# Optimization experiments

Measured on AMD Instinct MI355X. Metric: run time of the kernel, lower is better.

Reference implementation:

```python
import jax, jax.numpy as jnp
import numpy as np

LN_EPS = 1e-12
BIG = 1e30
BAND = 15  # end index may be at most 15 tokens after start


def output_layer(x, w1, b1, g, b, w2, b2):
    # Linear -> ReLU -> LayerNorm -> Linear (dropout is identity at eval)
    h = jax.nn.relu(x @ w1 + b1)
    mu = jnp.mean(h, axis=-1, keepdims=True)
    var = jnp.mean(jnp.square(h - mu), axis=-1, keepdims=True)
    h = (h - mu) * jax.lax.rsqrt(var + LN_EPS) * g + b
    return h @ w2 + b2


def setup_inputs() -> dict:
    key = jax.random.key(0)
    ks = jax.random.split(key, 8)
    B, S, D = 8, 4096, 1024
    H2 = 2 * D
    inp = {
        "context_input": jax.random.normal(ks[0], (B, S, D), jnp.float32),
        "context_mask": jnp.ones((B, S), jnp.float32),
    }
    def head(k1, k2, n_ans):
        return (
            0.02 * jax.random.normal(k1, (D, H2), jnp.float32),
            jnp.zeros((H2,), jnp.float32),
            jnp.ones((H2,), jnp.float32),
            jnp.zeros((H2,), jnp.float32),
            0.02 * jax.random.normal(k2, (H2, n_ans), jnp.float32),
            jnp.zeros((n_ans,), jnp.float32),
        )
    for name, k1, k2, n_ans in [("start", ks[1], ks[2], 1), ("end", ks[3], ks[4], 1), ("type", ks[5], ks[6], 4)]:
        w1, b1, g, b, w2, b2 = head(k1, k2, n_ans)
        inp[f"{name}_w1"] = w1; inp[f"{name}_b1"] = b1
        inp[f"{name}_g"] = g; inp[f"{name}_b"] = b
        inp[f"{name}_w2"] = w2; inp[f"{name}_b2"] = b2
    return inp


def reference(context_input, context_mask,
              start_w1, start_b1, start_g, start_b, start_w2, start_b2,
              end_w1, end_b1, end_g, end_b, end_w2, end_b2,
              type_w1, type_b1, type_g, type_b, type_w2, type_b2):
    S = context_input.shape[1]
    start_pred = output_layer(context_input, start_w1, start_b1, start_g, start_b, start_w2, start_b2)[..., 0] \
        - BIG * (1.0 - context_mask)  # [B,S]
    end_pred = output_layer(context_input, end_w1, end_b1, end_g, end_b, end_w2, end_b2)[..., 0] \
        - BIG * (1.0 - context_mask)  # [B,S]
    type_pred = output_layer(context_input[:, 0, :], type_w1, type_b1, type_g, type_b, type_w2, type_b2)  # [B,4]

    # outer[b,i,j] = start[b,i] + end[b,j], masked to band 0 <= j-i <= 15
    outer = start_pred[:, :, None] + end_pred[:, None, :]  # [B,S,S]
    i = jnp.arange(S)[:, None]
    j = jnp.arange(S)[None, :]
    band = ((j >= i) & (j <= i + BAND)).astype(outer.dtype)  # [S,S]
    outer = outer - BIG * (1.0 - band)[None]

    yp1 = jnp.argmax(jnp.max(outer, axis=2), axis=1)  # best start index [B]
    yp2 = jnp.argmax(jnp.max(outer, axis=1), axis=1)  # best end index [B]
    return start_pred, end_pred, type_pred, yp1, yp2
```

## Files before the change

kernel.cpp:

```cpp
#include <hip/hip_runtime.h>

typedef _Float16 f16x8 __attribute__((ext_vector_type(8)));
typedef float f32x4 __attribute__((ext_vector_type(4)));

#define BIGF 1e30f
#define M_TOT 32768
#define H2 2048

#define WS_XH 0u
#define WS_WT 67108864u
#define WS_BVEC 75497472u
#define WS_GW2 75513856u
#define WS_CONSTS 75530240u
#define WS_PART 75530496u
#define WS_TPART 100696320u

__global__ void k_convert_x(const float* __restrict__ x, _Float16* __restrict__ xh) {
  size_t i = ((size_t)blockIdx.x * 256 + threadIdx.x) * 8;
  float4 v0 = *(const float4*)(x + i);
  float4 v1 = *(const float4*)(x + i + 4);
  f16x8 h;
  h[0] = (_Float16)v0.x; h[1] = (_Float16)v0.y; h[2] = (_Float16)v0.z; h[3] = (_Float16)v0.w;
  h[4] = (_Float16)v1.x; h[5] = (_Float16)v1.y; h[6] = (_Float16)v1.z; h[7] = (_Float16)v1.w;
  *(f16x8*)(xh + i) = h;
}

__global__ void k_convert_w(const float* __restrict__ w_s, const float* __restrict__ w_e,
                            _Float16* __restrict__ wt) {
  __shared__ float tile[64][65];
  const float* w = blockIdx.z ? w_e : w_s;
  int n0 = blockIdx.x * 64, k0 = blockIdx.y * 64;
  int tx = threadIdx.x & 63, ty = threadIdx.x >> 6;
#pragma unroll
  for (int i = ty; i < 64; i += 4) tile[i][tx] = w[(size_t)(k0 + i) * H2 + n0 + tx];
  __syncthreads();
#pragma unroll
  for (int i = ty; i < 64; i += 4) {
    wt[((size_t)(blockIdx.z * H2 + n0 + i)) * 1024 + k0 + tx] = (_Float16)tile[tx][i];
  }
}

__global__ void k_pack(const float* __restrict__ s_b1, const float* __restrict__ s_g,
                       const float* __restrict__ s_w2, const float* __restrict__ e_b1,
                       const float* __restrict__ e_g, const float* __restrict__ e_w2,
                       float* __restrict__ bvec, float* __restrict__ gw2) {
  int i = blockIdx.x * 256 + threadIdx.x;
  int head = i >> 11, j = i & (H2 - 1);
  bvec[i] = head ? e_b1[j] : s_b1[j];
  gw2[i] = head ? e_g[j] * e_w2[j] : s_g[j] * s_w2[j];
}

__global__ void k_consts(const float* __restrict__ s_g, const float* __restrict__ s_b,
                         const float* __restrict__ s_w2, const float* __restrict__ s_b2,
                         const float* __restrict__ e_g, const float* __restrict__ e_b,
                         const float* __restrict__ e_w2, const float* __restrict__ e_b2,
                         float* __restrict__ consts) {
  int h = blockIdx.x;
  const float* g = h ? e_g : s_g;
  const float* b = h ? e_b : s_b;
  const float* w2 = h ? e_w2 : s_w2;
  const float* b2 = h ? e_b2 : s_b2;
  float c1 = 0.f, c2 = 0.f;
  for (int j = threadIdx.x; j < H2; j += 256) {
    float w = w2[j];
    c1 += g[j] * w;
    c2 += b[j] * w;
  }
  for (int m = 1; m < 64; m <<= 1) { c1 += __shfl_xor(c1, m); c2 += __shfl_xor(c2, m); }
  __shared__ float r1[4], r2[4];
  int wid = threadIdx.x >> 6;
  if ((threadIdx.x & 63) == 0) { r1[wid] = c1; r2[wid] = c2; }
  __syncthreads();
  if (threadIdx.x == 0) {
    consts[h * 2 + 0] = r1[0] + r1[1] + r1[2] + r1[3];
    consts[h * 2 + 1] = r2[0] + r2[1] + r2[2] + r2[3] + b2[0];
  }
}

#define BUF 65536
#define STA(q, tile, bufo)                                                              \
  __builtin_amdgcn_global_load_lds(                                                     \
      (const __attribute__((address_space(1))) unsigned int*)(srcA + (size_t)(q) * 131072 + (size_t)(tile) * 128), \
      (__attribute__((address_space(3))) unsigned int*)(lds + (bufo) + (q) * 8192 + t * 16), 16, 0, 0)
#define STB(q, tile, bufo)                                                              \
  __builtin_amdgcn_global_load_lds(                                                     \
      (const __attribute__((address_space(1))) unsigned int*)(srcB + (size_t)(q) * 131072 + (size_t)(tile) * 128), \
      (__attribute__((address_space(3))) unsigned int*)(lds + (bufo) + 32768 + (q) * 8192 + t * 16), 16, 0, 0)

#define READA(AF, mi0, BUFO)                                                            \
  AF[0][0] = *(const f16x8*)(lds + (BUFO) + arow + (mi0) * 2048 + low0);                \
  AF[0][1] = *(const f16x8*)(lds + (BUFO) + arow + (mi0) * 2048 + low1);                \
  AF[1][0] = *(const f16x8*)(lds + (BUFO) + arow + ((mi0) + 1) * 2048 + low0);          \
  AF[1][1] = *(const f16x8*)(lds + (BUFO) + arow + ((mi0) + 1) * 2048 + low1);

#define READB(BF, BUFO)                                                                 \
  _Pragma("unroll")                                                                     \
  for (int nj = 0; nj < 4; ++nj) {                                                      \
    BF[nj][0] = *(const f16x8*)(lds + (BUFO) + brow + nj * 2048 + low0);                \
    BF[nj][1] = *(const f16x8*)(lds + (BUFO) + brow + nj * 2048 + low1);                \
  }

#define MFMA2(m0, m1, AF, BF)                                                           \
  __builtin_amdgcn_s_setprio(1);                                                        \
  _Pragma("unroll")                                                                     \
  for (int nj = 0; nj < 4; ++nj) {                                                      \
    acc[m0][nj] = __builtin_amdgcn_mfma_f32_16x16x32_f16(AF[0][0], BF[nj][0], acc[m0][nj], 0, 0, 0); \
    acc[m1][nj] = __builtin_amdgcn_mfma_f32_16x16x32_f16(AF[1][0], BF[nj][0], acc[m1][nj], 0, 0, 0); \
  }                                                                                     \
  _Pragma("unroll")                                                                     \
  for (int nj = 0; nj < 4; ++nj) {                                                      \
    acc[m0][nj] = __builtin_amdgcn_mfma_f32_16x16x32_f16(AF[0][1], BF[nj][1], acc[m0][nj], 0, 0, 0); \
    acc[m1][nj] = __builtin_amdgcn_mfma_f32_16x16x32_f16(AF[1][1], BF[nj][1], acc[m1][nj], 0, 0, 0); \
  }                                                                                     \
  __builtin_amdgcn_s_setprio(0);

#define K_ITER(g, OB, OBN, BFC, BFN)                                                    \
  {                                                                                     \
                           \
    READA(afB, 2, OB);                                                                  \
    if ((g) < 15) { STA(1, (g) + 1, OBN); STA(3, (g) + 1, OBN); }                       \
    asm volatile("s_waitcnt lgkmcnt(4)" ::: "memory");                                  \
    __builtin_amdgcn_s_barrier();                                                       \
    __builtin_amdgcn_sched_barrier(0);                                                  \
    MFMA2(0, 1, afA, BFC);                                                              \
                           \
    READA(afA, 4, OB);                                                                  \
    if ((g) < 14) { STB(0, (g) + 2, OB); STB(1, (g) + 2, OB); }                         \
    asm volatile("s_waitcnt lgkmcnt(4)" ::: "memory");                                  \
    __builtin_amdgcn_s_barrier();                                                       \
    __builtin_amdgcn_sched_barrier(0);                                                  \
    MFMA2(2, 3, afB, BFC);                                                              \
           \
    READA(afB, 6, OB);                                                                  \
    if ((g) < 14) { STB(2, (g) + 2, OB); STB(3, (g) + 2, OB); }                         \
    if ((g) < 14)       asm volatile("s_waitcnt vmcnt(4)" ::: "memory");                \
    else if ((g) == 14) asm volatile("s_waitcnt vmcnt(0)" ::: "memory");                \
    asm volatile("s_waitcnt lgkmcnt(4)" ::: "memory");                                  \
    __builtin_amdgcn_s_barrier();                                                       \
    __builtin_amdgcn_sched_barrier(0);                                                  \
    MFMA2(4, 5, afA, BFC);                                                              \
       \
    if ((g) < 15) {                                                                     \
      READB(BFN, OBN);                                                                  \
      READA(afA, 0, OBN);                                                               \
      if ((g) < 14) { STA(0, (g) + 2, OB); STA(2, (g) + 2, OB); }                       \
      asm volatile("s_waitcnt lgkmcnt(12)" ::: "memory");                               \
    } else {                                                                            \
      asm volatile("s_waitcnt lgkmcnt(0)" ::: "memory");                                \
    }                                                                                   \
    __builtin_amdgcn_s_barrier();                                                       \
    __builtin_amdgcn_sched_barrier(0);                                                  \
    MFMA2(6, 7, afB, BFC);                                                              \
  }

__global__ __launch_bounds__(512, 2) void k_gemm(const _Float16* __restrict__ Xh,
                                                 const _Float16* __restrict__ Wt,
                                                 const float* __restrict__ bvec,
                                                 const float* __restrict__ gw2,
                                                 float* __restrict__ partials) {
  __shared__ char lds[2 * BUF];
  const int nb = blockIdx.x;
  const int mb = blockIdx.y;
  const int t = threadIdx.x;
  const int lane = t & 63, wid = t >> 6;
  const int c15 = lane & 15, g4 = lane >> 4;
  const int wmg = wid >> 2;
  const int wn = (wid & 3) * 64;

  f32x4 acc[8][4];
#pragma unroll
  for (int i = 0; i < 8; ++i)
#pragma unroll
    for (int j = 0; j < 4; ++j) acc[i][j] = (f32x4){0.f, 0.f, 0.f, 0.f};

  const char* Abase = (const char*)(Xh + (size_t)mb * 256 * 1024);
  const char* Bbase = (const char*)(Wt + (size_t)nb * 256 * 1024);
  const int rowl = t >> 3;
  const int swz = ((t & 7) * 16) ^ ((rowl & 7) << 4);
  const char* srcA = Abase + (size_t)rowl * 2048 + swz;
  const char* srcB = Bbase + (size_t)rowl * 2048 + swz;

  const int xorv = (c15 & 7) << 4;
  const int low0 = (g4 * 16) ^ xorv;
  const int low1 = (64 + g4 * 16) ^ xorv;
  const int arow = (wmg * 128 + c15) * 128;
  const int brow = 32768 + (wn + c15) * 128;

  STA(0, 0, 0); STA(1, 0, 0); STA(2, 0, 0); STA(3, 0, 0);
  STB(0, 0, 0); STB(1, 0, 0); STB(2, 0, 0); STB(3, 0, 0);
  STB(0, 1, BUF); STB(1, 1, BUF); STB(2, 1, BUF); STB(3, 1, BUF);
  STA(0, 1, BUF); STA(2, 1, BUF);
  asm volatile("s_waitcnt vmcnt(6)" ::: "memory");
  __builtin_amdgcn_s_barrier();
  __builtin_amdgcn_sched_barrier(0);

  f16x8 afA[2][2], afB[2][2], bfA[4][2], bfB[4][2];
  READB(bfA, 0);
  READA(afA, 0, 0);

#pragma unroll
  for (int gp = 0; gp < 8; ++gp) {
    K_ITER(2 * gp, 0u, BUF, bfA, bfB);
    K_ITER(2 * gp + 1, BUF, 0u, bfB, bfA);
  }

  float bv[4], gv[4];
#pragma unroll
  for (int nj = 0; nj < 4; ++nj) {
    int col = nb * 256 + wn + nj * 16 + c15;
    bv[nj] = bvec[col];
    gv[nj] = gw2[col];
  }
  const int slice = nb * 4 + (wid & 3);
#pragma unroll
  for (int mi = 0; mi < 8; ++mi) {
#pragma unroll
    for (int r = 0; r < 4; ++r) {
      float s1 = 0.f, s2 = 0.f, s3 = 0.f;
#pragma unroll
      for (int nj = 0; nj < 4; ++nj) {
        float v = acc[mi][nj][r] + bv[nj];
        v = fmaxf(v, 0.f);
        s1 += v;
        s2 += v * v;
        s3 += v * gv[nj];
      }
#pragma unroll
      for (int m = 1; m < 16; m <<= 1) {
        s1 += __shfl_xor(s1, m);
        s2 += __shfl_xor(s2, m);
        s3 += __shfl_xor(s3, m);
      }
      if (c15 == 0) {
        int rowg = mb * 256 + wmg * 128 + mi * 16 + g4 * 4 + r;
        partials[((size_t)(slice * 3 + 0)) * M_TOT + rowg] = s1;
        partials[((size_t)(slice * 3 + 1)) * M_TOT + rowg] = s2;
        partials[((size_t)(slice * 3 + 2)) * M_TOT + rowg] = s3;
      }
    }
  }
}

__global__ void k_reduce(const float* __restrict__ partials, const float* __restrict__ consts,
                         const float* __restrict__ mask, float* __restrict__ out) {
  int m = blockIdx.x * 256 + threadIdx.x;
  float s1 = 0.f, s2 = 0.f, s3 = 0.f, e1 = 0.f, e2 = 0.f, e3 = 0.f;
  for (int nb2 = 0; nb2 < 32; ++nb2) {
    s1 += partials[((size_t)(nb2 * 3 + 0)) * M_TOT + m];
    s2 += partials[((size_t)(nb2 * 3 + 1)) * M_TOT + m];
    s3 += partials[((size_t)(nb2 * 3 + 2)) * M_TOT + m];
  }
  for (int nb2 = 32; nb2 < 64; ++nb2) {
    e1 += partials[((size_t)(nb2 * 3 + 0)) * M_TOT + m];
    e2 += partials[((size_t)(nb2 * 3 + 1)) * M_TOT + m];
    e3 += partials[((size_t)(nb2 * 3 + 2)) * M_TOT + m];
  }
  const float H = (float)H2;
  float mu = s1 / H;
  float var = fmaxf(s2 / H - mu * mu, 0.f);
  float rs = 1.f / sqrtf(var + 1e-12f);
  float score_s = rs * (s3 - mu * consts[0]) + consts[1];
  mu = e1 / H;
  var = fmaxf(e2 / H - mu * mu, 0.f);
  rs = 1.f / sqrtf(var + 1e-12f);
  float score_e = rs * (e3 - mu * consts[2]) + consts[3];
  float mk = BIGF * (1.f - mask[m]);
  out[m] = score_s - mk;
  out[M_TOT + m] = score_e - mk;
}

__global__ void k_type_partial(const float* __restrict__ X, const float* __restrict__ w1,
                               const float* __restrict__ b1, const float* __restrict__ g,
                               const float* __restrict__ w2, float* __restrict__ tpart) {
  __shared__ float xs[1024];
  int cb = blockIdx.x, tok = blockIdx.y, t = threadIdx.x;
  const float* xp = X + (size_t)tok * 4096 * 1024;
  for (int i = t; i < 1024; i += 256) xs[i] = xp[i];
  __syncthreads();
  int j = cb * 256 + t;
  float dot = 0.f;
  for (int k = 0; k < 1024; ++k) dot += xs[k] * w1[(size_t)k * H2 + j];
  float h = fmaxf(dot + b1[j], 0.f);
  float gj = g[j];
  float s[6];
  s[0] = h;
  s[1] = h * h;
#pragma unroll
  for (int c = 0; c < 4; ++c) s[2 + c] = h * gj * w2[j * 4 + c];
  for (int m = 1; m < 64; m <<= 1)
#pragma unroll
    for (int q = 0; q < 6; ++q) s[q] += __shfl_xor(s[q], m);
  __shared__ float red[4][6];
  int wid = t >> 6;
  if ((t & 63) == 0)
#pragma unroll
    for (int q = 0; q < 6; ++q) red[wid][q] = s[q];
  __syncthreads();
  if (t == 0)
#pragma unroll
    for (int q = 0; q < 6; ++q)
      tpart[(tok * 8 + cb) * 6 + q] = red[0][q] + red[1][q] + red[2][q] + red[3][q];
}

__global__ void k_type_final(const float* __restrict__ tpart, const float* __restrict__ g,
                             const float* __restrict__ bb, const float* __restrict__ w2,
                             const float* __restrict__ b2, float* __restrict__ out) {
  int t = threadIdx.x;
  float c1[4] = {0.f, 0.f, 0.f, 0.f}, c2[4] = {0.f, 0.f, 0.f, 0.f};
  for (int j = t; j < H2; j += 256) {
    float gj = g[j], bj = bb[j];
#pragma unroll
    for (int c = 0; c < 4; ++c) {
      float w = w2[j * 4 + c];
      c1[c] += gj * w;
      c2[c] += bj * w;
    }
  }
  for (int m = 1; m < 64; m <<= 1)
#pragma unroll
    for (int c = 0; c < 4; ++c) { c1[c] += __shfl_xor(c1[c], m); c2[c] += __shfl_xor(c2[c], m); }
  __shared__ float rC1[4][4], rC2[4][4];
  int wid = t >> 6;
  if ((t & 63) == 0)
#pragma unroll
    for (int c = 0; c < 4; ++c) { rC1[wid][c] = c1[c]; rC2[wid][c] = c2[c]; }
  __syncthreads();
  __shared__ float sC1[4], sC2[4];
  if (t < 4) {
    sC1[t] = rC1[0][t] + rC1[1][t] + rC1[2][t] + rC1[3][t];
    sC2[t] = rC2[0][t] + rC2[1][t] + rC2[2][t] + rC2[3][t];
  }
  __syncthreads();
  if (t < 32) {
    int tok = t >> 2, c = t & 3;
    float s1 = 0.f, s2 = 0.f, s3 = 0.f;
    for (int cb = 0; cb < 8; ++cb) {
      s1 += tpart[(tok * 8 + cb) * 6 + 0];
      s2 += tpart[(tok * 8 + cb) * 6 + 1];
      s3 += tpart[(tok * 8 + cb) * 6 + 2 + c];
    }
    float mu = s1 / (float)H2;
    float var = fmaxf(s2 / (float)H2 - mu * mu, 0.f);
    float rs = 1.f / sqrtf(var + 1e-12f);
    out[65536 + tok * 4 + c] = rs * (s3 - mu * sC1[c]) + sC2[c] + b2[c];
  }
}

__global__ void k_band(const float* __restrict__ preds, float* __restrict__ out) {
  __shared__ float ss[4096], se[4096];
  int b = blockIdx.x, t = threadIdx.x;
  for (int i = t; i < 4096; i += 256) {
    ss[i] = preds[(size_t)b * 4096 + i];
    se[i] = preds[M_TOT + (size_t)b * 4096 + i];
  }
  __syncthreads();
  float bv1 = -3.0e38f, bv2 = -3.0e38f;
  int bi1 = 0x7fffffff, bi2 = 0x7fffffff;
  for (int i = t; i < 4096; i += 256) {
    float m1 = -3.0e38f;
    int jmax = i + 15 < 4095 ? i + 15 : 4095;
    for (int j = i; j <= jmax; ++j) m1 = fmaxf(m1, se[j]);
    float v1 = ss[i] + m1;
    if (v1 > bv1 || (v1 == bv1 && i < bi1)) { bv1 = v1; bi1 = i; }
    float m2 = -3.0e38f;
    int imin = i - 15 > 0 ? i - 15 : 0;
    for (int j = imin; j <= i; ++j) m2 = fmaxf(m2, ss[j]);
    float v2 = se[i] + m2;
    if (v2 > bv2 || (v2 == bv2 && i < bi2)) { bv2 = v2; bi2 = i; }
  }
  for (int m = 1; m < 64; m <<= 1) {
    float ov = __shfl_xor(bv1, m);
    int oi = __shfl_xor(bi1, m);
    if (ov > bv1 || (ov == bv1 && oi < bi1)) { bv1 = ov; bi1 = oi; }
    ov = __shfl_xor(bv2, m);
    oi = __shfl_xor(bi2, m);
    if (ov > bv2 || (ov == bv2 && oi < bi2)) { bv2 = ov; bi2 = oi; }
  }
  __shared__ float rv[2][4];
  __shared__ int ri[2][4];
  int wid = t >> 6;
  if ((t & 63) == 0) { rv[0][wid] = bv1; ri[0][wid] = bi1; rv[1][wid] = bv2; ri[1][wid] = bi2; }
  __syncthreads();
  if (t == 0) {
    float v = rv[0][0];
    int ix = ri[0][0];
    for (int w = 1; w < 4; ++w)
      if (rv[0][w] > v || (rv[0][w] == v && ri[0][w] < ix)) { v = rv[0][w]; ix = ri[0][w]; }
    out[65568 + b] = (float)ix;
    v = rv[1][0];
    ix = ri[1][0];
    for (int w = 1; w < 4; ++w)
      if (rv[1][w] > v || (rv[1][w] == v && ri[1][w] < ix)) { v = rv[1][w]; ix = ri[1][w]; }
    out[65576 + b] = (float)ix;
  }
}

extern "C" void kernel_launch(void* const* d_in, const int* in_sizes, int n_in, void* d_out,
                              int out_size, void* d_ws, size_t ws_size, hipStream_t stream) {
  const float* X = (const float*)d_in[0];
  const float* mask = (const float*)d_in[1];
  const float* s_w1 = (const float*)d_in[2];
  const float* s_b1 = (const float*)d_in[3];
  const float* s_g = (const float*)d_in[4];
  const float* s_b = (const float*)d_in[5];
  const float* s_w2 = (const float*)d_in[6];
  const float* s_b2 = (const float*)d_in[7];
  const float* e_w1 = (const float*)d_in[8];
  const float* e_b1 = (const float*)d_in[9];
  const float* e_g = (const float*)d_in[10];
  const float* e_b = (const float*)d_in[11];
  const float* e_w2 = (const float*)d_in[12];
  const float* e_b2 = (const float*)d_in[13];
  const float* t_w1 = (const float*)d_in[14];
  const float* t_b1 = (const float*)d_in[15];
  const float* t_g = (const float*)d_in[16];
  const float* t_b = (const float*)d_in[17];
  const float* t_w2 = (const float*)d_in[18];
  const float* t_b2 = (const float*)d_in[19];

  char* ws = (char*)d_ws;
  _Float16* Xh = (_Float16*)(ws + WS_XH);
  _Float16* Wt = (_Float16*)(ws + WS_WT);
  float* bvec = (float*)(ws + WS_BVEC);
  float* gw2 = (float*)(ws + WS_GW2);
  float* consts = (float*)(ws + WS_CONSTS);
  float* partials = (float*)(ws + WS_PART);
  float* tpart = (float*)(ws + WS_TPART);
  float* out = (float*)d_out;

  k_convert_x<<<16384, 256, 0, stream>>>(X, Xh);
  k_convert_w<<<dim3(32, 16, 2), 256, 0, stream>>>(s_w1, e_w1, Wt);
  k_pack<<<16, 256, 0, stream>>>(s_b1, s_g, s_w2, e_b1, e_g, e_w2, bvec, gw2);
  k_consts<<<2, 256, 0, stream>>>(s_g, s_b, s_w2, s_b2, e_g, e_b, e_w2, e_b2, consts);
  k_gemm<<<dim3(16, 128), 512, 0, stream>>>(Xh, Wt, bvec, gw2, partials);
  k_reduce<<<128, 256, 0, stream>>>(partials, consts, mask, out);
  k_type_partial<<<dim3(8, 8), 256, 0, stream>>>(X, t_w1, t_b1, t_g, t_w2, tpart);
  k_type_final<<<1, 256, 0, stream>>>(tpart, t_g, t_b, t_w2, t_b2, out);
  k_band<<<8, 256, 0, stream>>>(out, out);
}
```

Measured before the change: 428.9 us.

## Simplify GEMM K-loop pipeline, swizzle block order, merge prep kernels

```diff
diff --git a/kernel.cpp b/kernel.cpp
--- a/kernel.cpp
+++ b/kernel.cpp
@@ -40,44 +40,44 @@
   }
 }
 
-__global__ void k_pack(const float* __restrict__ s_b1, const float* __restrict__ s_g,
-                       const float* __restrict__ s_w2, const float* __restrict__ e_b1,
+__global__ void k_prep(const float* __restrict__ s_b1, const float* __restrict__ s_g,
+                       const float* __restrict__ s_w2, const float* __restrict__ s_b,
+                       const float* __restrict__ s_b2, const float* __restrict__ e_b1,
                        const float* __restrict__ e_g, const float* __restrict__ e_w2,
-                       float* __restrict__ bvec, float* __restrict__ gw2) {
-  int i = blockIdx.x * 256 + threadIdx.x;
-  int head = i >> 11, j = i & (H2 - 1);
-  bvec[i] = head ? e_b1[j] : s_b1[j];
-  gw2[i] = head ? e_g[j] * e_w2[j] : s_g[j] * s_w2[j];
-}
-
-__global__ void k_consts(const float* __restrict__ s_g, const float* __restrict__ s_b,
-                         const float* __restrict__ s_w2, const float* __restrict__ s_b2,
-                         const float* __restrict__ e_g, const float* __restrict__ e_b,
-                         const float* __restrict__ e_w2, const float* __restrict__ e_b2,
-                         float* __restrict__ consts) {
-  int h = blockIdx.x;
-  const float* g = h ? e_g : s_g;
-  const float* b = h ? e_b : s_b;
-  const float* w2 = h ? e_w2 : s_w2;
-  const float* b2 = h ? e_b2 : s_b2;
-  float c1 = 0.f, c2 = 0.f;
-  for (int j = threadIdx.x; j < H2; j += 256) {
-    float w = w2[j];
-    c1 += g[j] * w;
-    c2 += b[j] * w;
-  }
-  for (int m = 1; m < 64; m <<= 1) { c1 += __shfl_xor(c1, m); c2 += __shfl_xor(c2, m); }
-  __shared__ float r1[4], r2[4];
-  int wid = threadIdx.x >> 6;
-  if ((threadIdx.x & 63) == 0) { r1[wid] = c1; r2[wid] = c2; }
-  __syncthreads();
-  if (threadIdx.x == 0) {
-    consts[h * 2 + 0] = r1[0] + r1[1] + r1[2] + r1[3];
-    consts[h * 2 + 1] = r2[0] + r2[1] + r2[2] + r2[3] + b2[0];
-  }
-}
-
-#define BUF 65536
+                       const float* __restrict__ e_b, const float* __restrict__ e_b2,
+                       float* __restrict__ bvec, float* __restrict__ gw2,
+                       float* __restrict__ consts) {
+  int blk = blockIdx.x;
+  if (blk < 16) {
+    int i = blk * 256 + threadIdx.x;
+    int head = i >> 11, j = i & (H2 - 1);
+    bvec[i] = head ? e_b1[j] : s_b1[j];
+    gw2[i] = head ? e_g[j] * e_w2[j] : s_g[j] * s_w2[j];
+  } else {
+    int h = blk - 16;
+    const float* g = h ? e_g : s_g;
+    const float* b = h ? e_b : s_b;
+    const float* w2 = h ? e_w2 : s_w2;
+    const float* b2 = h ? e_b2 : s_b2;
+    float c1 = 0.f, c2 = 0.f;
+    for (int j = threadIdx.x; j < H2; j += 256) {
+      float w = w2[j];
+      c1 += g[j] * w;
+      c2 += b[j] * w;
+    }
+    for (int m = 1; m < 64; m <<= 1) { c1 += __shfl_xor(c1, m); c2 += __shfl_xor(c2, m); }
+    __shared__ float r1[4], r2[4];
+    int wid = threadIdx.x >> 6;
+    if ((threadIdx.x & 63) == 0) { r1[wid] = c1; r2[wid] = c2; }
+    __syncthreads();
+    if (threadIdx.x == 0) {
+      consts[h * 2 + 0] = r1[0] + r1[1] + r1[2] + r1[3];
+      consts[h * 2 + 1] = r2[0] + r2[1] + r2[2] + r2[3] + b2[0];
+    }
+  }
+}
+
+#define BUF 65536u
 #define STA(q, tile, bufo)                                                              \
   __builtin_amdgcn_global_load_lds(                                                     \
       (const __attribute__((address_space(1))) unsigned int*)(srcA + (size_t)(q) * 131072 + (size_t)(tile) * 128), \
@@ -85,7 +85,7 @@
 #define STB(q, tile, bufo)                                                              \
   __builtin_amdgcn_global_load_lds(                                                     \
       (const __attribute__((address_space(1))) unsigned int*)(srcB + (size_t)(q) * 131072 + (size_t)(tile) * 128), \
-      (__attribute__((address_space(3))) unsigned int*)(lds + (bufo) + 32768 + (q) * 8192 + t * 16), 16, 0, 0)
+      (__attribute__((address_space(3))) unsigned int*)(lds + (bufo) + 32768u + (q) * 8192 + t * 16), 16, 0, 0)
 
 #define READA(AF, mi0, BUFO)                                                            \
   AF[0][0] = *(const f16x8*)(lds + (BUFO) + arow + (mi0) * 2048 + low0);                \
@@ -114,44 +114,11 @@
   }                                                                                     \
   __builtin_amdgcn_s_setprio(0);
 
-#define K_ITER(g, OB, OBN, BFC, BFN)                                                    \
-  {                                                                                     \
-                           \
-    READA(afB, 2, OB);                                                                  \
-    if ((g) < 15) { STA(1, (g) + 1, OBN); STA(3, (g) + 1, OBN); }                       \
-    asm volatile("s_waitcnt lgkmcnt(4)" ::: "memory");                                  \
-    __builtin_amdgcn_s_barrier();                                                       \
-    __builtin_amdgcn_sched_barrier(0);                                                  \
-    MFMA2(0, 1, afA, BFC);                                                              \
-                           \
-    READA(afA, 4, OB);                                                                  \
-    if ((g) < 14) { STB(0, (g) + 2, OB); STB(1, (g) + 2, OB); }                         \
-    asm volatile("s_waitcnt lgkmcnt(4)" ::: "memory");                                  \
-    __builtin_amdgcn_s_barrier();                                                       \
-    __builtin_amdgcn_sched_barrier(0);                                                  \
-    MFMA2(2, 3, afB, BFC);                                                              \
-           \
-    READA(afB, 6, OB);                                                                  \
-    if ((g) < 14) { STB(2, (g) + 2, OB); STB(3, (g) + 2, OB); }                         \
-    if ((g) < 14)       asm volatile("s_waitcnt vmcnt(4)" ::: "memory");                \
-    else if ((g) == 14) asm volatile("s_waitcnt vmcnt(0)" ::: "memory");                \
-    asm volatile("s_waitcnt lgkmcnt(4)" ::: "memory");                                  \
-    __builtin_amdgcn_s_barrier();                                                       \
-    __builtin_amdgcn_sched_barrier(0);                                                  \
-    MFMA2(4, 5, afA, BFC);                                                              \
-       \
-    if ((g) < 15) {                                                                     \
-      READB(BFN, OBN);                                                                  \
-      READA(afA, 0, OBN);                                                               \
-      if ((g) < 14) { STA(0, (g) + 2, OB); STA(2, (g) + 2, OB); }                       \
-      asm volatile("s_waitcnt lgkmcnt(12)" ::: "memory");                               \
-    } else {                                                                            \
-      asm volatile("s_waitcnt lgkmcnt(0)" ::: "memory");                                \
-    }                                                                                   \
-    __builtin_amdgcn_s_barrier();                                                       \
-    __builtin_amdgcn_sched_barrier(0);                                                  \
-    MFMA2(6, 7, afB, BFC);                                                              \
-  }
+#define PHASE_TAIL                                                                      \
+  __builtin_amdgcn_sched_barrier(0);                                                    \
+  __builtin_amdgcn_s_barrier();                                                         \
+  asm volatile("s_waitcnt lgkmcnt(0)" ::: "memory");                                    \
+  __builtin_amdgcn_sched_barrier(0);
 
 __global__ __launch_bounds__(512, 2) void k_gemm(const _Float16* __restrict__ Xh,
                                                  const _Float16* __restrict__ Wt,
@@ -159,8 +126,10 @@
                                                  const float* __restrict__ gw2,
                                                  float* __restrict__ partials) {
   __shared__ char lds[2 * BUF];
-  const int nb = blockIdx.x;
-  const int mb = blockIdx.y;
+  const int bid = blockIdx.x;
+  const int swzb = (bid & 7) * 256 + (bid >> 3);
+  const int nb = swzb & 15;
+  const int mb = swzb >> 4;
   const int t = threadIdx.x;
   const int lane = t & 63, wid = t >> 6;
   const int c15 = lane & 15, g4 = lane >> 4;
@@ -194,14 +163,32 @@
   __builtin_amdgcn_s_barrier();
   __builtin_amdgcn_sched_barrier(0);
 
-  f16x8 afA[2][2], afB[2][2], bfA[4][2], bfB[4][2];
-  READB(bfA, 0);
-  READA(afA, 0, 0);
-
-#pragma unroll
-  for (int gp = 0; gp < 8; ++gp) {
-    K_ITER(2 * gp, 0u, BUF, bfA, bfB);
-    K_ITER(2 * gp + 1, BUF, 0u, bfB, bfA);
+  f16x8 af[2][2], bf[4][2];
+
+#pragma unroll
+  for (int g = 0; g < 16; ++g) {
+    const unsigned OB = (unsigned)(g & 1) * BUF;
+    const unsigned ON = OB ^ BUF;
+    READB(bf, OB);
+    READA(af, 0, OB);
+    if (g < 15) { STA(1, g + 1, ON); STA(3, g + 1, ON); }
+    PHASE_TAIL
+    MFMA2(0, 1, af, bf);
+    READA(af, 2, OB);
+    if (g < 14) { STB(0, g + 2, OB); STB(1, g + 2, OB); }
+    PHASE_TAIL
+    MFMA2(2, 3, af, bf);
+    READA(af, 4, OB);
+    if (g < 14) { STB(2, g + 2, OB); STB(3, g + 2, OB); }
+    PHASE_TAIL
+    MFMA2(4, 5, af, bf);
+    READA(af, 6, OB);
+    if (g < 14) { STA(0, g + 2, OB); STA(2, g + 2, OB); }
+    PHASE_TAIL
+    MFMA2(6, 7, af, bf);
+    if (g < 14) asm volatile("s_waitcnt vmcnt(6)" ::: "memory");
+    else        asm volatile("s_waitcnt vmcnt(0)" ::: "memory");
+    __builtin_amdgcn_s_barrier();
   }
 
   float bv[4], gv[4];
@@ -430,9 +417,9 @@
 
   k_convert_x<<<16384, 256, 0, stream>>>(X, Xh);
   k_convert_w<<<dim3(32, 16, 2), 256, 0, stream>>>(s_w1, e_w1, Wt);
-  k_pack<<<16, 256, 0, stream>>>(s_b1, s_g, s_w2, e_b1, e_g, e_w2, bvec, gw2);
-  k_consts<<<2, 256, 0, stream>>>(s_g, s_b, s_w2, s_b2, e_g, e_b, e_w2, e_b2, consts);
-  k_gemm<<<dim3(16, 128), 512, 0, stream>>>(Xh, Wt, bvec, gw2, partials);
+  k_prep<<<18, 256, 0, stream>>>(s_b1, s_g, s_w2, s_b, s_b2, e_b1, e_g, e_w2, e_b, e_b2,
+                                 bvec, gw2, consts);
+  k_gemm<<<2048, 512, 0, stream>>>(Xh, Wt, bvec, gw2, partials);
   k_reduce<<<128, 256, 0, stream>>>(partials, consts, mask, out);
   k_type_partial<<<dim3(8, 8), 256, 0, stream>>>(X, t_w1, t_b1, t_g, t_w2, tpart);
   k_type_final<<<1, 256, 0, stream>>>(tpart, t_g, t_b, t_w2, t_b2, out);
```

Result: no change. 422.9 us (-1.4%).

## Reduce GEMM epilogue partials in LDS per block and merge prep kernels

Applied to the files above, without the earlier changes.

```diff
diff --git a/kernel.cpp b/kernel.cpp
--- a/kernel.cpp
+++ b/kernel.cpp
@@ -40,40 +40,40 @@
   }
 }
 
-__global__ void k_pack(const float* __restrict__ s_b1, const float* __restrict__ s_g,
-                       const float* __restrict__ s_w2, const float* __restrict__ e_b1,
+__global__ void k_prep(const float* __restrict__ s_b1, const float* __restrict__ s_g,
+                       const float* __restrict__ s_w2, const float* __restrict__ s_b,
+                       const float* __restrict__ s_b2, const float* __restrict__ e_b1,
                        const float* __restrict__ e_g, const float* __restrict__ e_w2,
-                       float* __restrict__ bvec, float* __restrict__ gw2) {
-  int i = blockIdx.x * 256 + threadIdx.x;
-  int head = i >> 11, j = i & (H2 - 1);
-  bvec[i] = head ? e_b1[j] : s_b1[j];
-  gw2[i] = head ? e_g[j] * e_w2[j] : s_g[j] * s_w2[j];
-}
-
-__global__ void k_consts(const float* __restrict__ s_g, const float* __restrict__ s_b,
-                         const float* __restrict__ s_w2, const float* __restrict__ s_b2,
-                         const float* __restrict__ e_g, const float* __restrict__ e_b,
-                         const float* __restrict__ e_w2, const float* __restrict__ e_b2,
-                         float* __restrict__ consts) {
-  int h = blockIdx.x;
-  const float* g = h ? e_g : s_g;
-  const float* b = h ? e_b : s_b;
-  const float* w2 = h ? e_w2 : s_w2;
-  const float* b2 = h ? e_b2 : s_b2;
-  float c1 = 0.f, c2 = 0.f;
-  for (int j = threadIdx.x; j < H2; j += 256) {
-    float w = w2[j];
-    c1 += g[j] * w;
-    c2 += b[j] * w;
-  }
-  for (int m = 1; m < 64; m <<= 1) { c1 += __shfl_xor(c1, m); c2 += __shfl_xor(c2, m); }
-  __shared__ float r1[4], r2[4];
-  int wid = threadIdx.x >> 6;
-  if ((threadIdx.x & 63) == 0) { r1[wid] = c1; r2[wid] = c2; }
-  __syncthreads();
-  if (threadIdx.x == 0) {
-    consts[h * 2 + 0] = r1[0] + r1[1] + r1[2] + r1[3];
-    consts[h * 2 + 1] = r2[0] + r2[1] + r2[2] + r2[3] + b2[0];
+                       const float* __restrict__ e_b, const float* __restrict__ e_b2,
+                       float* __restrict__ bvec, float* __restrict__ gw2,
+                       float* __restrict__ consts) {
+  int blk = blockIdx.x;
+  if (blk < 16) {
+    int i = blk * 256 + threadIdx.x;
+    int head = i >> 11, j = i & (H2 - 1);
+    bvec[i] = head ? e_b1[j] : s_b1[j];
+    gw2[i] = head ? e_g[j] * e_w2[j] : s_g[j] * s_w2[j];
+  } else {
+    int h = blk - 16;
+    const float* g = h ? e_g : s_g;
+    const float* b = h ? e_b : s_b;
+    const float* w2 = h ? e_w2 : s_w2;
+    const float* b2 = h ? e_b2 : s_b2;
+    float c1 = 0.f, c2 = 0.f;
+    for (int j = threadIdx.x; j < H2; j += 256) {
+      float w = w2[j];
+      c1 += g[j] * w;
+      c2 += b[j] * w;
+    }
+    for (int m = 1; m < 64; m <<= 1) { c1 += __shfl_xor(c1, m); c2 += __shfl_xor(c2, m); }
+    __shared__ float r1[4], r2[4];
+    int wid = threadIdx.x >> 6;
+    if ((threadIdx.x & 63) == 0) { r1[wid] = c1; r2[wid] = c2; }
+    __syncthreads();
+    if (threadIdx.x == 0) {
+      consts[h * 2 + 0] = r1[0] + r1[1] + r1[2] + r1[3];
+      consts[h * 2 + 1] = r2[0] + r2[1] + r2[2] + r2[3] + b2[0];
+    }
   }
 }
 
@@ -165,7 +165,8 @@
   const int lane = t & 63, wid = t >> 6;
   const int c15 = lane & 15, g4 = lane >> 4;
   const int wmg = wid >> 2;
-  const int wn = (wid & 3) * 64;
+  const int wq = wid & 3;
+  const int wn = wq * 64;
 
   f32x4 acc[8][4];
 #pragma unroll
@@ -204,6 +205,9 @@
     K_ITER(2 * gp + 1, BUF, 0u, bfB, bfA);
   }
 
+  __syncthreads();
+  float* red = (float*)lds;
+
   float bv[4], gv[4];
 #pragma unroll
   for (int nj = 0; nj < 4; ++nj) {
@@ -211,7 +215,6 @@
     bv[nj] = bvec[col];
     gv[nj] = gw2[col];
   }
-  const int slice = nb * 4 + (wid & 3);
 #pragma unroll
   for (int mi = 0; mi < 8; ++mi) {
 #pragma unroll
@@ -232,12 +235,23 @@
         s3 += __shfl_xor(s3, m);
       }
       if (c15 == 0) {
-        int rowg = mb * 256 + wmg * 128 + mi * 16 + g4 * 4 + r;
-        partials[((size_t)(slice * 3 + 0)) * M_TOT + rowg] = s1;
-        partials[((size_t)(slice * 3 + 1)) * M_TOT + rowg] = s2;
-        partials[((size_t)(slice * 3 + 2)) * M_TOT + rowg] = s3;
+        int row = mi * 16 + g4 * 4 + r;
+        float* p = red + (((wmg * 4 + wq) * 128 + row) * 3);
+        p[0] = s1; p[1] = s2; p[2] = s3;
       }
     }
+  }
+  __syncthreads();
+  for (int idx = t; idx < 768; idx += 512) {
+    int wmgi = idx / 384;
+    int rem = idx - wmgi * 384;
+    int row = rem / 3, k = rem - row * 3;
+    float s = red[((wmgi * 4 + 0) * 128 + row) * 3 + k] +
+              red[((wmgi * 4 + 1) * 128 + row) * 3 + k] +
+              red[((wmgi * 4 + 2) * 128 + row) * 3 + k] +
+              red[((wmgi * 4 + 3) * 128 + row) * 3 + k];
+    int rowg = mb * 256 + wmgi * 128 + row;
+    partials[((size_t)(nb * 3 + k)) * M_TOT + rowg] = s;
   }
 }
 
@@ -245,15 +259,15 @@
                          const float* __restrict__ mask, float* __restrict__ out) {
   int m = blockIdx.x * 256 + threadIdx.x;
   float s1 = 0.f, s2 = 0.f, s3 = 0.f, e1 = 0.f, e2 = 0.f, e3 = 0.f;
-  for (int nb2 = 0; nb2 < 32; ++nb2) {
-    s1 += partials[((size_t)(nb2 * 3 + 0)) * M_TOT + m];
-    s2 += partials[((size_t)(nb2 * 3 + 1)) * M_TOT + m];
-    s3 += partials[((size_t)(nb2 * 3 + 2)) * M_TOT + m];
-  }
-  for (int nb2 = 32; nb2 < 64; ++nb2) {
-    e1 += partials[((size_t)(nb2 * 3 + 0)) * M_TOT + m];
-    e2 += partials[((size_t)(nb2 * 3 + 1)) * M_TOT + m];
-    e3 += partials[((size_t)(nb2 * 3 + 2)) * M_TOT + m];
+  for (int nb = 0; nb < 8; ++nb) {
+    s1 += partials[((size_t)(nb * 3 + 0)) * M_TOT + m];
+    s2 += partials[((size_t)(nb * 3 + 1)) * M_TOT + m];
+    s3 += partials[((size_t)(nb * 3 + 2)) * M_TOT + m];
+  }
+  for (int nb = 8; nb < 16; ++nb) {
+    e1 += partials[((size_t)(nb * 3 + 0)) * M_TOT + m];
+    e2 += partials[((size_t)(nb * 3 + 1)) * M_TOT + m];
+    e3 += partials[((size_t)(nb * 3 + 2)) * M_TOT + m];
   }
   const float H = (float)H2;
   float mu = s1 / H;
@@ -430,8 +444,8 @@
 
   k_convert_x<<<16384, 256, 0, stream>>>(X, Xh);
   k_convert_w<<<dim3(32, 16, 2), 256, 0, stream>>>(s_w1, e_w1, Wt);
-  k_pack<<<16, 256, 0, stream>>>(s_b1, s_g, s_w2, e_b1, e_g, e_w2, bvec, gw2);
-  k_consts<<<2, 256, 0, stream>>>(s_g, s_b, s_w2, s_b2, e_g, e_b, e_w2, e_b2, consts);
+  k_prep<<<18, 256, 0, stream>>>(s_b1, s_g, s_w2, s_b, s_b2, e_b1, e_g, e_w2, e_b, e_b2,
+                                 bvec, gw2, consts);
   k_gemm<<<dim3(16, 128), 512, 0, stream>>>(Xh, Wt, bvec, gw2, partials);
   k_reduce<<<128, 256, 0, stream>>>(partials, consts, mask, out);
   k_type_partial<<<dim3(8, 8), 256, 0, stream>>>(X, t_w1, t_b1, t_g, t_w2, tpart);
```

Result: faster. 403.7 us (-5.9%).
